# Kernel optimization log

Hardware: AMD Instinct MI355X
Metric: run time of the kernel (lower is better)

## Reference

```python
import jax, jax.numpy as jnp
import numpy as np

B, L, D = 2, 1024, 1024
H, KV, CH = 16, 4, 8          # attn heads, kv heads, context-manager heads
HD = D // H                   # 64
E, K, FF = 8, 2, 4 * D        # experts, top-k, ffn hidden
DC = 4                        # conv kernel size
EPS = 1e-6


def setup_inputs() -> dict:
    key = jax.random.key(0)
    ks = jax.random.split(key, 32)
    s = 0.02
    n = lambda k, shp: jax.random.normal(k, shp, jnp.float32) * s
    return {
        'x': jax.random.normal(ks[0], (B, L, D), jnp.float32),
        'mask': jnp.ones((B, L), jnp.int32),
        'w_rms1': jnp.ones((D,), jnp.float32),
        'w_rms2': jnp.ones((D,), jnp.float32),
        'w_rms3': jnp.ones((D,), jnp.float32),
        'w_rms4': jnp.ones((D,), jnp.float32),
        'Wq': n(ks[1], (D, D)), 'Wk': n(ks[2], (D, KV * HD)),
        'Wv': n(ks[3], (D, KV * HD)), 'Wo': n(ks[4], (D, D)),
        'Cq': n(ks[5], (D, D)), 'Ck': n(ks[6], (D, D)),
        'Cv': n(ks[7], (D, D)), 'Co': n(ks[8], (D, D)),
        'Wi': n(ks[9], (D, 2 * D)), 'bi': jnp.zeros((2 * D,), jnp.float32),
        'conv_w': n(ks[10], (D, 1, DC)), 'conv_b': jnp.zeros((D,), jnp.float32),
        'Wod': n(ks[11], (D, D)), 'bod': jnp.zeros((D,), jnp.float32),
        'w_gate': n(ks[12], (E, D)),
        'W1': n(ks[13], (E, D, FF)), 'b1': jnp.zeros((E, FF), jnp.float32),
        'W2': n(ks[14], (E, FF, D)), 'b2': jnp.zeros((E, D), jnp.float32),
    }


def _rmsnorm(x, w):
    rms = jnp.sqrt(jnp.mean(x * x, axis=-1, keepdims=True) + EPS)
    return w * (x / rms)


def _mha(x, mask, Wq, Wk, Wv, Wo, nh, nkv):
    b, l, d = x.shape
    hd = d // nh
    q = (x @ Wq).reshape(b, l, nh, hd)
    k = (x @ Wk).reshape(b, l, nkv, hd)
    v = (x @ Wv).reshape(b, l, nkv, hd)
    if nh != nkv:
        rep = nh // nkv
        k = jnp.repeat(k, rep, axis=2)
        v = jnp.repeat(v, rep, axis=2)
    scores = jnp.einsum('bqhd,bkhd->bhqk', q, k) * (hd ** -0.5)
    scores = jnp.where(mask[:, None, None, :] == 0, -jnp.inf, scores)
    attn = jax.nn.softmax(scores, axis=-1)
    out = jnp.einsum('bhqk,bkhd->bqhd', attn, v).reshape(b, l, d)
    return out @ Wo


def _deltanet(x, Wi, bi, conv_w, conv_b, Wod, bod):
    gv = x @ Wi + bi
    gate, value = jnp.split(gv, 2, axis=-1)
    # depthwise causal conv1d (kernel DC, left pad DC-1, truncated to L)
    v_ncl = jnp.transpose(value, (0, 2, 1))  # [B, D, L]
    conv = jax.lax.conv_general_dilated(
        v_ncl, conv_w, window_strides=(1,), padding=[(DC - 1, 0)],
        feature_group_count=D, dimension_numbers=('NCH', 'OIH', 'NCH'))
    conv = conv + conv_b[None, :, None]
    conv = jnp.transpose(conv, (0, 2, 1))  # [B, L, D]
    gated = conv * jax.nn.silu(gate)
    return gated @ Wod + bod


def _moe(x, w_gate, W1, b1, W2, b2):
    b, l, d = x.shape
    flat = x.reshape(-1, d)                                  # [T, D]
    gate = jax.nn.softmax(flat @ w_gate.T, axis=-1)          # [T, E]
    topk_scores, topk_idx = jax.lax.top_k(gate, K)           # [T, K]
    onehot = jax.nn.one_hot(topk_idx, E, dtype=flat.dtype)   # [T, K, E]
    combine = jnp.sum(topk_scores[..., None] * onehot, axis=1)  # [T, E]
    h = jnp.einsum('td,edh->teh', flat, W1) + b1
    h = jax.nn.gelu(h, approximate=False)
    y = jnp.einsum('teh,ehd->ted', h, W2) + b2
    out = jnp.einsum('ted,te->td', y, combine)
    return out.reshape(b, l, d)


def reference(x, mask, w_rms1, w_rms2, w_rms3, w_rms4,
              Wq, Wk, Wv, Wo, Cq, Ck, Cv, Co,
              Wi, bi, conv_w, conv_b, Wod, bod,
              w_gate, W1, b1, W2, b2):
    # eval mode: dropout = identity. multi_token_pred output is discarded by the block.
    res1 = x
    h = _rmsnorm(x, w_rms1)
    h = res1 + _mha(h, mask, Wq, Wk, Wv, Wo, H, KV)
    res2 = h
    # ContextManager stand-in: 8-head softmax self-attention (source unavailable)
    cm = _mha(h, mask, Cq, Ck, Cv, Co, CH, CH)
    h = res2 + cm
    res3 = h
    g = _rmsnorm(h, w_rms2)
    h = res3 + _deltanet(g, Wi, bi, conv_w, conv_b, Wod, bod)
    res4 = h
    g = _rmsnorm(h, w_rms3)
    h = res4 + _moe(g, w_gate, W1, b1, W2, b2)
    h = _rmsnorm(h, w_rms4)
    return h
```

## Files before the change

### kernel.cpp

```cpp
#include <hip/hip_runtime.h>
#include <hip/hip_bf16.h>
#include <math.h>

#define T_TOK 2048
#define B_SZ 2
#define L_SEQ 1024
#define D_MOD 1024
#define N_H 16
#define N_KV 4
#define N_CH 8
#define N_E 8
#define FF_DIM 4096
#define DC_K 4
#define EPS_F 1e-6f

typedef unsigned short u16;
typedef unsigned int u32;
typedef short s16x8 __attribute__((ext_vector_type(8)));
typedef u16 u16x8 __attribute__((ext_vector_type(8)));
typedef float f32x4 __attribute__((ext_vector_type(4)));
struct alignas(8) U16x4 { u16 a, b, c, d; };

__device__ __forceinline__ float gelu_exact(float x) {
    return 0.5f * x * (1.0f + erff(x * 0.70710678118654752f));
}
__device__ __forceinline__ u16 f2bf(float f) {
    u32 x = __float_as_uint(f);
    return (u16)((x + 0x7fffu + ((x >> 16) & 1u)) >> 16);
}
__device__ __forceinline__ float b2f(u16 u) {
    return __uint_as_float(((u32)u) << 16);
}
__device__ __forceinline__ void gload_lds16(const u16* g, u16* l) {
    __builtin_amdgcn_global_load_lds(
        (const __attribute__((address_space(1))) u32*)g,
        (__attribute__((address_space(3))) u32*)l, 16, 0, 0);
}

struct TDesc {
    const float* src;
    u16* dst;
    int R, C, dstStride, dstRowOff, tileBase, nPerMat;
};
struct TPack { TDesc d[12]; };

__global__ __launch_bounds__(256) void transpose_all(TPack p, int nTiles) {
    __shared__ float ts[64][65];
    int tid = threadIdx.x;
    int t = blockIdx.x;
    float4 rg[4];
    u16* dstB = nullptr;
    int dstStr = 0;

    auto prep = [&](int tt) {
        int i = 0;
#pragma unroll
        for (int j = 1; j < 12; ++j)
            if (tt >= p.d[j].tileBase) i = j;
        TDesc d = p.d[i];
        int local = tt - d.tileBase;
        int e = local / d.nPerMat;
        local -= e * d.nPerMat;
        int ntx = d.C >> 6;
        int bx = local % ntx, by = local / ntx;
        const float* src = d.src + (size_t)e * d.R * d.C + (size_t)(by * 64) * d.C + bx * 64;
#pragma unroll
        for (int k = 0; k < 4; ++k) {
            int fidx = k * 256 + tid;
            int r = fidx >> 4, c4 = (fidx & 15) << 2;
            rg[k] = *(const float4*)(src + (size_t)r * d.C + c4);
        }
        dstB = d.dst + (size_t)e * d.C * d.dstStride +
               (size_t)(d.dstRowOff + bx * 64) * d.dstStride + by * 64;
        dstStr = d.dstStride;
    };

    if (t < nTiles) prep(t);
    for (; t < nTiles; t += gridDim.x) {
#pragma unroll
        for (int k = 0; k < 4; ++k) {
            int fidx = k * 256 + tid;
            int r = fidx >> 4, c4 = (fidx & 15) << 2;
            ts[r][c4] = rg[k].x;
            ts[r][c4 + 1] = rg[k].y;
            ts[r][c4 + 2] = rg[k].z;
            ts[r][c4 + 3] = rg[k].w;
        }
        u16* db = dstB;
        int dstr = dstStr;
        __syncthreads();
        int tn = t + gridDim.x;
        if (tn < nTiles) prep(tn);
#pragma unroll
        for (int k = 0; k < 2; ++k) {
            int idx = k * 256 + tid;
            int c = idx >> 3, r8 = (idx & 7) << 3;
            u16x8 o;
#pragma unroll
            for (int j = 0; j < 8; ++j) o[j] = f2bf(ts[r8 + j][c]);
            *(u16x8*)(db + (size_t)c * dstr + r8) = o;
        }
        __syncthreads();
    }
}

__global__ __launch_bounds__(256) void rmsnorm_kernel(const float* __restrict__ x,
                                                      const float* __restrict__ w,
                                                      float* __restrict__ fo,
                                                      u16* __restrict__ bo) {
    int row = blockIdx.x;
    int tid = threadIdx.x;
    const float* xr = x + (size_t)row * D_MOD;
    float4 v = ((const float4*)xr)[tid];
    float ss = v.x * v.x + v.y * v.y + v.z * v.z + v.w * v.w;
    __shared__ float red[256];
    red[tid] = ss;
    __syncthreads();
    for (int s = 128; s > 0; s >>= 1) {
        if (tid < s) red[tid] += red[tid + s];
        __syncthreads();
    }
    float inv = 1.0f / sqrtf(red[0] * (1.0f / D_MOD) + EPS_F);
    float4 wv = ((const float4*)w)[tid];
    float4 o;
    o.x = v.x * inv * wv.x;
    o.y = v.y * inv * wv.y;
    o.z = v.z * inv * wv.z;
    o.w = v.w * inv * wv.w;
    if (fo) ((float4*)(fo + (size_t)row * D_MOD))[tid] = o;
    if (bo) {
        U16x4 b;
        b.a = f2bf(o.x); b.b = f2bf(o.y); b.c = f2bf(o.z); b.d = f2bf(o.w);
        *(U16x4*)(bo + (size_t)row * D_MOD + tid * 4) = b;
    }
}

template <int MODE, int GELU, int OUTF, int OUTB, int BM>
__global__ __launch_bounds__(256) void mfma_gemm(const u16* __restrict__ A,
                                                 const u16* __restrict__ BT,
                                                 const float* __restrict__ bias,
                                                 const float* __restrict__ res,
                                                 float* __restrict__ C,
                                                 u16* __restrict__ Cb,
                                                 const int* __restrict__ list,
                                                 const int* __restrict__ offs,
                                                 const int* __restrict__ counts,
                                                 int M, int N, int K, int nx) {
    constexpr int PWR = BM / 2;
    constexpr int MI = PWR / 16;
    constexpr int NI = 4;
    constexpr int NAI = (BM >= 64) ? (BM / 64) : 1;
    __shared__ u16 ldsA[2][BM * 32];
    __shared__ u16 ldsB[2][128 * 32];
    int tid = threadIdx.x;
    int lane = tid & 63, w = tid >> 6;
    int wr = w >> 1, wc = w & 1;
    int bx, by, e;
    if (MODE == 0) {
        bx = blockIdx.x; by = blockIdx.y; e = 0;
    } else {
        int id = blockIdx.x;
        e = id & 7;
        int r = id >> 3;
        bx = r % nx;
        by = r / nx;
    }
    int cnt, off;
    if (MODE == 0) { cnt = M; off = 0; }
    else { cnt = counts[e]; off = offs[e]; }
    int m0 = by * BM;
    if (m0 >= cnt) return;
    int n0 = bx * 128;
    const u16* Bt = BT + (size_t)e * (size_t)N * K;

    const u16* aSrc[NAI];
    const u16* bSrc[2];
#pragma unroll
    for (int j = 0; j < NAI; ++j) {
        int rowA = (BM >= 64) ? (j * 64 + w * 16 + (lane >> 2))
                              : (w * 16 + (lane >> 2));
        int slot = lane & 3;
        int rl = m0 + ((rowA < BM) ? rowA : (BM - 1));
        if (rl >= cnt) rl = cnt - 1;
        size_t ga;
        if (MODE == 1) ga = (size_t)list[off + rl] * K;
        else if (MODE == 2) ga = (size_t)(off + rl) * K;
        else ga = (size_t)rl * K;
        aSrc[j] = A + ga + ((slot ^ ((rowA >> 1) & 3)) << 3);
    }
#pragma unroll
    for (int j = 0; j < 2; ++j) {
        int rowB = j * 64 + w * 16 + (lane >> 2);
        int slot = lane & 3;
        bSrc[j] = Bt + (size_t)(n0 + rowB) * K + ((slot ^ ((rowB >> 1) & 3)) << 3);
    }

    auto stage = [&](int buf, int k0) {
        if constexpr (BM == 32) {
            if (w < 2) gload_lds16(aSrc[0] + k0, &ldsA[buf][w * 512]);
        } else {
#pragma unroll
            for (int j = 0; j < NAI; ++j)
                gload_lds16(aSrc[j] + k0, &ldsA[buf][(j * 256 + w * 64) * 8]);
        }
#pragma unroll
        for (int j = 0; j < 2; ++j)
            gload_lds16(bSrc[j] + k0, &ldsB[buf][(j * 256 + w * 64) * 8]);
    };

    f32x4 acc[MI][NI] = {};
    int r16 = lane & 15, cr = lane >> 4;

    stage(0, 0);
    __syncthreads();
    int cur = 0;
    for (int k0 = 0; k0 < K; k0 += 32) {
        if (k0 + 32 < K) stage(cur ^ 1, k0 + 32);
        s16x8 af[MI], bfr[NI];
#pragma unroll
        for (int mi = 0; mi < MI; ++mi) {
            int row = wr * PWR + mi * 16 + r16;
            af[mi] = *(const s16x8*)&ldsA[cur][row * 32 + ((cr ^ ((row >> 1) & 3)) << 3)];
        }
#pragma unroll
        for (int ni = 0; ni < NI; ++ni) {
            int row = wc * 64 + ni * 16 + r16;
            bfr[ni] = *(const s16x8*)&ldsB[cur][row * 32 + ((cr ^ ((row >> 1) & 3)) << 3)];
        }
#pragma unroll
        for (int mi = 0; mi < MI; ++mi)
#pragma unroll
            for (int ni = 0; ni < NI; ++ni)
                acc[mi][ni] = __builtin_amdgcn_mfma_f32_16x16x32_bf16(af[mi], bfr[ni],
                                                                      acc[mi][ni], 0, 0, 0);
        __syncthreads();
        cur ^= 1;
    }

    const float* bias_e = bias ? (bias + (MODE ? (size_t)e * N : 0)) : nullptr;
#pragma unroll
    for (int mi = 0; mi < MI; ++mi) {
#pragma unroll
        for (int ni = 0; ni < NI; ++ni) {
            int rloc = wr * PWR + mi * 16 + (lane >> 4) * 4;
            int col = n0 + wc * 64 + ni * 16 + (lane & 15);
#pragma unroll
            for (int jj = 0; jj < 4; ++jj) {
                int rl = m0 + rloc + jj;
                if (rl >= cnt) continue;
                float val = acc[mi][ni][jj];
                if (bias_e) val += bias_e[col];
                if (GELU) val = gelu_exact(val);
                size_t crow = (MODE == 0) ? (size_t)rl : (size_t)(off + rl);
                if (res) val += res[crow * N + col];
                if (OUTF) C[crow * N + col] = val;
                if (OUTB) Cb[crow * N + col] = f2bf(val);
            }
        }
    }
}

template <int HD>
__global__ __launch_bounds__(256) void mfma_attn(const u16* __restrict__ Qb,
                                                 const u16* __restrict__ Kb,
                                                 const u16* __restrict__ Vb,
                                                 u16* __restrict__ O,
                                                 int stride, int ostride,
                                                 int nh, int nkv, float scale) {
    constexpr int KT = 64;
    constexpr int CH = HD / 8;
    constexpr int NF = HD / 32;
    constexpr int ND = HD / 16;
    constexpr int VSTR = 72;
    constexpr int NISS = (64 * CH) / (64 * 4);

    __shared__ u16 Kl[64 * HD];
    __shared__ u16 Vt[HD * VSTR];
    __shared__ u16 Pl[4][16 * 72];

    int tid = threadIdx.x, lane = tid & 63, w = tid >> 6;
    int g = lane >> 4, r16 = lane & 15;
    int q0 = blockIdx.x * 64, h = blockIdx.y, b = blockIdx.z;
    int kvh = h / (nh / nkv);

    const u16* Qp = Qb + (size_t)(b * L_SEQ + q0 + w * 16 + r16) * stride + h * HD + g * 8;
    s16x8 qf[NF];
#pragma unroll
    for (int f = 0; f < NF; ++f) qf[f] = *(const s16x8*)(Qp + f * 32);

    const u16* Kbase = Kb + (size_t)(b * L_SEQ) * stride + (size_t)kvh * HD;
    const u16* Vbase = Vb + (size_t)(b * L_SEQ) * stride + (size_t)kvh * HD;

    int srcOffK[NISS];
#pragma unroll
    for (int i = 0; i < NISS; ++i) {
        int ci = (w * NISS + i) * 64 + lane;
        int row = ci / CH;
        int ch = ci % CH;
        srcOffK[i] = row * stride + ((ch ^ (row & 7)) << 3);
    }

    f32x4 ofr[ND] = {};
    float m_r[4], l_r[4];
#pragma unroll
    for (int r = 0; r < 4; ++r) { m_r[r] = -1e30f; l_r[r] = 0.f; }

    for (int kt = 0; kt < L_SEQ / KT; ++kt) {
        const u16* Ksrc = Kbase + (size_t)(kt * KT) * stride;
        const u16* Vsrc = Vbase + (size_t)(kt * KT) * stride;
        __syncthreads();
#pragma unroll
        for (int i = 0; i < NISS; ++i)
            gload_lds16(Ksrc + srcOffK[i], Kl + (size_t)(w * NISS + i) * 512);
#pragma unroll
        for (int half = 0; half < HD / 64; ++half) {
            int dbase = w * 16 + half * 64;
            u16x8 v0 = *(const u16x8*)(Vsrc + (size_t)lane * stride + dbase);
            u16x8 v1 = *(const u16x8*)(Vsrc + (size_t)lane * stride + dbase + 8);
#pragma unroll
            for (int j = 0; j < 8; ++j) {
                Vt[(dbase + j) * VSTR + lane] = v0[j];
                Vt[(dbase + 8 + j) * VSTR + lane] = v1[j];
            }
        }
        __syncthreads();

        f32x4 s[4];
        __builtin_amdgcn_s_setprio(1);
#pragma unroll
        for (int sub = 0; sub < 4; ++sub) {
            f32x4 acc = {};
#pragma unroll
            for (int f = 0; f < NF; ++f) {
                int row = sub * 16 + r16;
                int chunk = (f * 4 + g) ^ (row & 7);
                s16x8 kf = *(const s16x8*)&Kl[(row * CH + chunk) * 8];
                acc = __builtin_amdgcn_mfma_f32_16x16x32_bf16(qf[f], kf, acc, 0, 0, 0);
            }
            s[sub] = acc;
        }
        __builtin_amdgcn_s_setprio(0);

#pragma unroll
        for (int sub = 0; sub < 4; ++sub)
#pragma unroll
            for (int r = 0; r < 4; ++r) s[sub][r] *= scale;
#pragma unroll
        for (int r = 0; r < 4; ++r) {
            float mx = fmaxf(fmaxf(s[0][r], s[1][r]), fmaxf(s[2][r], s[3][r]));
            mx = fmaxf(mx, __shfl_xor(mx, 1));
            mx = fmaxf(mx, __shfl_xor(mx, 2));
            mx = fmaxf(mx, __shfl_xor(mx, 4));
            mx = fmaxf(mx, __shfl_xor(mx, 8));
            float mo = m_r[r];
            float mn = fmaxf(mo, mx);
            float sc = __expf(mo - mn);
            m_r[r] = mn;
            float sum = 0.f;
#pragma unroll
            for (int sub = 0; sub < 4; ++sub) {
                float e = __expf(s[sub][r] - mn);
                s[sub][r] = e;
                sum += e;
            }
            sum += __shfl_xor(sum, 1);
            sum += __shfl_xor(sum, 2);
            sum += __shfl_xor(sum, 4);
            sum += __shfl_xor(sum, 8);
            l_r[r] = l_r[r] * sc + sum;
#pragma unroll
            for (int dsub = 0; dsub < ND; ++dsub) ofr[dsub][r] *= sc;
        }

        u16* Pw = Pl[w];
#pragma unroll
        for (int sub = 0; sub < 4; ++sub)
#pragma unroll
            for (int r = 0; r < 4; ++r) {
                int q = g * 4 + r;
                int k = sub * 16 + r16;
                Pw[q * 72 + (((k >> 3) ^ (q & 7)) << 3) + (k & 7)] = f2bf(s[sub][r]);
            }
        __syncthreads();

        s16x8 pf[2];
#pragma unroll
        for (int ks = 0; ks < 2; ++ks) {
            int chunk = (ks * 4 + g) ^ (r16 & 7);
            pf[ks] = *(const s16x8*)&Pw[r16 * 72 + chunk * 8];
        }
        __builtin_amdgcn_s_setprio(1);
#pragma unroll
        for (int dsub = 0; dsub < ND; ++dsub)
#pragma unroll
            for (int ks = 0; ks < 2; ++ks) {
                s16x8 vf = *(const s16x8*)&Vt[(dsub * 16 + r16) * VSTR + ks * 32 + g * 8];
                ofr[dsub] = __builtin_amdgcn_mfma_f32_16x16x32_bf16(pf[ks], vf, ofr[dsub], 0, 0, 0);
            }
        __builtin_amdgcn_s_setprio(0);
    }

    float inv[4];
#pragma unroll
    for (int r = 0; r < 4; ++r) inv[r] = 1.0f / l_r[r];
#pragma unroll
    for (int dsub = 0; dsub < ND; ++dsub)
#pragma unroll
        for (int r = 0; r < 4; ++r) {
            int q = q0 + w * 16 + g * 4 + r;
            O[(size_t)(b * L_SEQ + q) * ostride + h * HD + dsub * 16 + r16] =
                f2bf(ofr[dsub][r] * inv[r]);
        }
}

__global__ __launch_bounds__(256) void conv_gate_kernel(const u16* __restrict__ gv,
                                                        const float* __restrict__ cw,
                                                        const float* __restrict__ cb,
                                                        u16* __restrict__ gated) {
    int idx = blockIdx.x * 256 + threadIdx.x;
    if (idx >= T_TOK * D_MOD / 8) return;
    int d8 = (idx & 127) << 3;
    int t = idx >> 7;
    int l = t & (L_SEQ - 1);
    float conv[8];
#pragma unroll
    for (int j = 0; j < 8; ++j) conv[j] = cb[d8 + j];
#pragma unroll
    for (int i = 0; i < DC_K; ++i) {
        int lp = l - (DC_K - 1) + i;
        if (lp >= 0) {
            u16x8 v8 = *(const u16x8*)(gv + (size_t)(t - l + lp) * (2 * D_MOD) + D_MOD + d8);
#pragma unroll
            for (int j = 0; j < 8; ++j) conv[j] += b2f(v8[j]) * cw[(d8 + j) * DC_K + i];
        }
    }
    u16x8 g8 = *(const u16x8*)(gv + (size_t)t * (2 * D_MOD) + d8);
    u16x8 o;
#pragma unroll
    for (int j = 0; j < 8; ++j) {
        float gate = b2f(g8[j]);
        float sig = 1.0f / (1.0f + expf(-gate));
        o[j] = f2bf(conv[j] * (gate * sig));
    }
    *(u16x8*)(gated + (size_t)t * D_MOD + d8) = o;
}

__global__ __launch_bounds__(256) void route_kernel(const float* __restrict__ g,
                                                    const float* __restrict__ wg,
                                                    int* __restrict__ tIdx,
                                                    float* __restrict__ tScore,
                                                    int* __restrict__ counts) {
    int t = blockIdx.x, tid = threadIdx.x;
    __shared__ float gs[D_MOD];
    __shared__ float logits[N_E];
    ((float4*)gs)[tid] = ((const float4*)(g + (size_t)t * D_MOD))[tid];
    __syncthreads();
    int e = tid >> 5, lane = tid & 31;
    const float* w = wg + (size_t)e * D_MOD;
    float p = 0.f;
    for (int d = lane; d < D_MOD; d += 32) p += gs[d] * w[d];
    for (int o = 16; o > 0; o >>= 1) p += __shfl_down(p, o, 32);
    if (lane == 0) logits[e] = p;
    __syncthreads();
    if (tid == 0) {
        float mx = logits[0];
        for (int e2 = 1; e2 < N_E; ++e2) mx = fmaxf(mx, logits[e2]);
        float pe[N_E];
        float Z = 0.f;
        for (int e2 = 0; e2 < N_E; ++e2) {
            pe[e2] = expf(logits[e2] - mx);
            Z += pe[e2];
        }
        int i0 = 0;
        float b0 = pe[0];
        for (int e2 = 1; e2 < N_E; ++e2)
            if (pe[e2] > b0) { b0 = pe[e2]; i0 = e2; }
        int i1 = -1;
        float b1 = -1.f;
        for (int e2 = 0; e2 < N_E; ++e2)
            if (e2 != i0 && pe[e2] > b1) { b1 = pe[e2]; i1 = e2; }
        float invZ = 1.0f / Z;
        tIdx[t * 2] = i0;
        tIdx[t * 2 + 1] = i1;
        tScore[t * 2] = b0 * invZ;
        tScore[t * 2 + 1] = b1 * invZ;
        atomicAdd(&counts[i0], 1);
        atomicAdd(&counts[i1], 1);
    }
}

__global__ void prefix_kernel(const int* __restrict__ counts, int* __restrict__ offs,
                              int* __restrict__ cursor) {
    if (threadIdx.x == 0) {
        int acc = 0;
        for (int e = 0; e < N_E; ++e) {
            offs[e] = acc;
            acc += counts[e];
            cursor[e] = 0;
        }
    }
}

__global__ __launch_bounds__(256) void fill_kernel(const int* __restrict__ tIdx,
                                                   const int* __restrict__ offs,
                                                   int* __restrict__ cursor,
                                                   int* __restrict__ list,
                                                   int* __restrict__ pairRow) {
    int t = blockIdx.x * 256 + threadIdx.x;
    if (t >= T_TOK) return;
    for (int kk = 0; kk < 2; ++kk) {
        int e = tIdx[t * 2 + kk];
        int pos = atomicAdd(&cursor[e], 1);
        int slot = offs[e] + pos;
        list[slot] = t;
        pairRow[t * 2 + kk] = slot;
    }
}

__global__ __launch_bounds__(256) void combine_rms_kernel(const u16* __restrict__ ysel,
                                                          const float* __restrict__ tScore,
                                                          const int* __restrict__ pairRow,
                                                          const float* __restrict__ h,
                                                          const float* __restrict__ w,
                                                          float* __restrict__ out) {
    int row = blockIdx.x;
    int tid = threadIdx.x;
    float4 v = ((const float4*)(h + (size_t)row * D_MOD))[tid];
    int r0 = pairRow[row * 2], r1 = pairRow[row * 2 + 1];
    float s0 = tScore[row * 2], s1 = tScore[row * 2 + 1];
    U16x4 y0 = *(const U16x4*)(ysel + (size_t)r0 * D_MOD + tid * 4);
    U16x4 y1 = *(const U16x4*)(ysel + (size_t)r1 * D_MOD + tid * 4);
    v.x += s0 * b2f(y0.a) + s1 * b2f(y1.a);
    v.y += s0 * b2f(y0.b) + s1 * b2f(y1.b);
    v.z += s0 * b2f(y0.c) + s1 * b2f(y1.c);
    v.w += s0 * b2f(y0.d) + s1 * b2f(y1.d);
    __shared__ float red[256];
    red[tid] = v.x * v.x + v.y * v.y + v.z * v.z + v.w * v.w;
    __syncthreads();
    for (int s = 128; s > 0; s >>= 1) {
        if (tid < s) red[tid] += red[tid + s];
        __syncthreads();
    }
    float inv = 1.0f / sqrtf(red[0] * (1.0f / D_MOD) + EPS_F);
    float4 wv = ((const float4*)w)[tid];
    float4 o;
    o.x = v.x * inv * wv.x;
    o.y = v.y * inv * wv.y;
    o.z = v.z * inv * wv.z;
    o.w = v.w * inv * wv.w;
    ((float4*)(out + (size_t)row * D_MOD))[tid] = o;
}

extern "C" void kernel_launch(void* const* d_in, const int* in_sizes, int n_in,
                              void* d_out, int out_size, void* d_ws, size_t ws_size,
                              hipStream_t stream) {
    const float* x = (const float*)d_in[0];
    const float* w_rms1 = (const float*)d_in[2];
    const float* w_rms2 = (const float*)d_in[3];
    const float* w_rms3 = (const float*)d_in[4];
    const float* w_rms4 = (const float*)d_in[5];
    const float* Wq = (const float*)d_in[6];
    const float* Wk = (const float*)d_in[7];
    const float* Wv = (const float*)d_in[8];
    const float* Wo = (const float*)d_in[9];
    const float* Cq = (const float*)d_in[10];
    const float* Ck = (const float*)d_in[11];
    const float* Cv = (const float*)d_in[12];
    const float* Co = (const float*)d_in[13];
    const float* Wi = (const float*)d_in[14];
    const float* bi = (const float*)d_in[15];
    const float* conv_w = (const float*)d_in[16];
    const float* conv_b = (const float*)d_in[17];
    const float* Wod = (const float*)d_in[18];
    const float* bod = (const float*)d_in[19];
    const float* w_gate = (const float*)d_in[20];
    const float* W1 = (const float*)d_in[21];
    const float* b1 = (const float*)d_in[22];
    const float* W2 = (const float*)d_in[23];
    const float* b2 = (const float*)d_in[24];
    float* out = (float*)d_out;

    char* ws = (char*)d_ws;
    size_t off = 0;
    auto alloc_f = [&](size_t n) { float* p = (float*)(ws + off); off += n * 4; return p; };
    auto alloc_b = [&](size_t n) { u16* p = (u16*)(ws + off); off += n * 2; return p; };

    u16* qkvT = alloc_b((size_t)1536 * 1024);
    u16* cqkvT = alloc_b((size_t)3072 * 1024);
    u16* WoT = alloc_b((size_t)1024 * 1024);
    u16* CoT = alloc_b((size_t)1024 * 1024);
    u16* WiT = alloc_b((size_t)2048 * 1024);
    u16* WodT = alloc_b((size_t)1024 * 1024);
    u16* W1T = alloc_b((size_t)N_E * FF_DIM * 1024);
    u16* W2T = alloc_b((size_t)N_E * 1024 * FF_DIM);
    const size_t TD = (size_t)T_TOK * D_MOD;
    float* h = alloc_f(TD);
    float* nrm = alloc_f(TD);
    u16* nrm_bf = alloc_b(TD);
    u16* h_bf = alloc_b(TD);
    u16* ab_bf = alloc_b(TD);
    u16* qkv_bf = alloc_b((size_t)T_TOK * 3072);
    u16* gv_bf = alloc_b((size_t)T_TOK * 2048);
    u16* hsel = alloc_b((size_t)2 * T_TOK * FF_DIM);
    u16* ysel = alloc_b((size_t)2 * T_TOK * D_MOD);
    int* counts = (int*)(ws + off); off += N_E * 4;
    int* offs = (int*)(ws + off); off += N_E * 4;
    int* cursor = (int*)(ws + off); off += N_E * 4;
    int* tIdx = (int*)(ws + off); off += 2 * T_TOK * 4;
    int* list = (int*)(ws + off); off += 2 * T_TOK * 4;
    int* pairRow = (int*)(ws + off); off += 2 * T_TOK * 4;
    float* tScore = alloc_f(2 * T_TOK);

    TPack tp;
    int tb = 0;
    auto mkd = [&](int i, const float* s, u16* d, int R, int C, int ds, int ro, int nmat) {
        int per = (C >> 6) * (R >> 6);
        tp.d[i] = TDesc{s, d, R, C, ds, ro, tb, per};
        tb += per * nmat;
    };
    mkd(0, Wq, qkvT, 1024, 1024, 1024, 0, 1);
    mkd(1, Wk, qkvT, 1024, 256, 1024, 1024, 1);
    mkd(2, Wv, qkvT, 1024, 256, 1024, 1280, 1);
    mkd(3, Cq, cqkvT, 1024, 1024, 1024, 0, 1);
    mkd(4, Ck, cqkvT, 1024, 1024, 1024, 1024, 1);
    mkd(5, Cv, cqkvT, 1024, 1024, 1024, 2048, 1);
    mkd(6, Wo, WoT, 1024, 1024, 1024, 0, 1);
    mkd(7, Co, CoT, 1024, 1024, 1024, 0, 1);
    mkd(8, Wi, WiT, 1024, 2048, 1024, 0, 1);
    mkd(9, Wod, WodT, 1024, 1024, 1024, 0, 1);
    mkd(10, W1, W1T, 1024, FF_DIM, 1024, 0, N_E);
    mkd(11, W2, W2T, FF_DIM, 1024, FF_DIM, 0, N_E);
    transpose_all<<<2048, 256, 0, stream>>>(tp, tb);

    rmsnorm_kernel<<<T_TOK, 256, 0, stream>>>(x, w_rms1, nullptr, nrm_bf);
    mfma_gemm<0, 0, 0, 1, 32><<<dim3(12, 64, 1), 256, 0, stream>>>(
        nrm_bf, qkvT, nullptr, nullptr, nullptr, qkv_bf, nullptr, nullptr, nullptr,
        T_TOK, 1536, 1024, 0);
    mfma_attn<64><<<dim3(16, N_H, B_SZ), 256, 0, stream>>>(
        qkv_bf, qkv_bf + 1024, qkv_bf + 1280, ab_bf, 1536, 1024, N_H, N_KV, 0.125f);
    mfma_gemm<0, 0, 1, 1, 32><<<dim3(8, 64, 1), 256, 0, stream>>>(
        ab_bf, WoT, nullptr, x, h, h_bf, nullptr, nullptr, nullptr, T_TOK, 1024, 1024, 0);

    mfma_gemm<0, 0, 0, 1, 32><<<dim3(24, 64, 1), 256, 0, stream>>>(
        h_bf, cqkvT, nullptr, nullptr, nullptr, qkv_bf, nullptr, nullptr, nullptr,
        T_TOK, 3072, 1024, 0);
    mfma_attn<128><<<dim3(16, N_CH, B_SZ), 256, 0, stream>>>(
        qkv_bf, qkv_bf + 1024, qkv_bf + 2048, ab_bf, 3072, 1024, N_CH, N_CH,
        0.088388347648318447f);
    mfma_gemm<0, 0, 1, 0, 32><<<dim3(8, 64, 1), 256, 0, stream>>>(
        ab_bf, CoT, nullptr, h, h, nullptr, nullptr, nullptr, nullptr, T_TOK, 1024, 1024, 0);

    rmsnorm_kernel<<<T_TOK, 256, 0, stream>>>(h, w_rms2, nullptr, nrm_bf);
    mfma_gemm<0, 0, 0, 1, 32><<<dim3(16, 64, 1), 256, 0, stream>>>(
        nrm_bf, WiT, bi, nullptr, nullptr, gv_bf, nullptr, nullptr, nullptr, T_TOK, 2048, 1024, 0);
    conv_gate_kernel<<<(T_TOK * D_MOD / 8 + 255) / 256, 256, 0, stream>>>(gv_bf, conv_w, conv_b, ab_bf);
    mfma_gemm<0, 0, 1, 0, 32><<<dim3(8, 64, 1), 256, 0, stream>>>(
        ab_bf, WodT, bod, h, h, nullptr, nullptr, nullptr, nullptr, T_TOK, 1024, 1024, 0);

    rmsnorm_kernel<<<T_TOK, 256, 0, stream>>>(h, w_rms3, nrm, nrm_bf);
    hipMemsetAsync(counts, 0, N_E * sizeof(int), stream);
    route_kernel<<<T_TOK, 256, 0, stream>>>(nrm, w_gate, tIdx, tScore, counts);
    prefix_kernel<<<1, 64, 0, stream>>>(counts, offs, cursor);
    fill_kernel<<<(T_TOK + 255) / 256, 256, 0, stream>>>(tIdx, offs, cursor, list, pairRow);
    mfma_gemm<1, 1, 0, 1, 128><<<32 * 16 * 8, 256, 0, stream>>>(
        nrm_bf, W1T, b1, nullptr, nullptr, hsel, list, offs, counts, T_TOK, FF_DIM, 1024, 32);
    mfma_gemm<2, 0, 0, 1, 32><<<8 * 64 * 8, 256, 0, stream>>>(
        hsel, W2T, b2, nullptr, nullptr, ysel, list, offs, counts, T_TOK, 1024, FF_DIM, 8);
    combine_rms_kernel<<<T_TOK, 256, 0, stream>>>(ysel, tScore, pairRow, h, w_rms4, out);
}
```

Baseline: 650.6 us.

## Spread expert weight transposes across dense GEMM kernels as tail work

Takes the MoE W1/W2 fp32→bf16 transposes out of the upfront transpose kernel and splits their 16384 tiles across the five dense GEMM launches. Each GEMM block does its tile after finishing its matmul output, reusing the same shared memory. The aim is to fill idle slots left by the small dense GEMM grids so the large expert transpose is no longer a serial launch on its own. The trade-off is longer GEMM kernels and a larger shared memory footprint when the transpose buffer is bigger than the GEMM tiles. The hard-coded tile ranges must also add up exactly to the full set.

```diff
diff --git a/kernel.cpp b/kernel.cpp
--- a/kernel.cpp
+++ b/kernel.cpp
@@ -42,65 +42,41 @@
     u16* dst;
     int R, C, dstStride, dstRowOff, tileBase, nPerMat;
 };
-struct TPack { TDesc d[12]; };
-
-__global__ __launch_bounds__(256) void transpose_all(TPack p, int nTiles) {
+struct TPack { TDesc d[10]; };
+
+__global__ __launch_bounds__(256) void transpose_all(TPack p) {
     __shared__ float ts[64][65];
+    int t = blockIdx.x;
+    int i = 0;
+#pragma unroll
+    for (int j = 1; j < 10; ++j)
+        if (t >= p.d[j].tileBase) i = j;
+    TDesc d = p.d[i];
+    int local = t - d.tileBase;
+    int e = local / d.nPerMat;
+    local -= e * d.nPerMat;
+    int ntx = d.C >> 6;
+    int bx = local % ntx, by = local / ntx;
+    const float* src = d.src + (size_t)e * d.R * d.C + (size_t)(by * 64) * d.C + bx * 64;
+    u16* dst = d.dst + (size_t)e * d.C * d.dstStride +
+               (size_t)(d.dstRowOff + bx * 64) * d.dstStride + by * 64;
     int tid = threadIdx.x;
-    int t = blockIdx.x;
-    float4 rg[4];
-    u16* dstB = nullptr;
-    int dstStr = 0;
-
-    auto prep = [&](int tt) {
-        int i = 0;
-#pragma unroll
-        for (int j = 1; j < 12; ++j)
-            if (tt >= p.d[j].tileBase) i = j;
-        TDesc d = p.d[i];
-        int local = tt - d.tileBase;
-        int e = local / d.nPerMat;
-        local -= e * d.nPerMat;
-        int ntx = d.C >> 6;
-        int bx = local % ntx, by = local / ntx;
-        const float* src = d.src + (size_t)e * d.R * d.C + (size_t)(by * 64) * d.C + bx * 64;
-#pragma unroll
-        for (int k = 0; k < 4; ++k) {
-            int fidx = k * 256 + tid;
-            int r = fidx >> 4, c4 = (fidx & 15) << 2;
-            rg[k] = *(const float4*)(src + (size_t)r * d.C + c4);
-        }
-        dstB = d.dst + (size_t)e * d.C * d.dstStride +
-               (size_t)(d.dstRowOff + bx * 64) * d.dstStride + by * 64;
-        dstStr = d.dstStride;
-    };
-
-    if (t < nTiles) prep(t);
-    for (; t < nTiles; t += gridDim.x) {
-#pragma unroll
-        for (int k = 0; k < 4; ++k) {
-            int fidx = k * 256 + tid;
-            int r = fidx >> 4, c4 = (fidx & 15) << 2;
-            ts[r][c4] = rg[k].x;
-            ts[r][c4 + 1] = rg[k].y;
-            ts[r][c4 + 2] = rg[k].z;
-            ts[r][c4 + 3] = rg[k].w;
-        }
-        u16* db = dstB;
-        int dstr = dstStr;
-        __syncthreads();
-        int tn = t + gridDim.x;
-        if (tn < nTiles) prep(tn);
-#pragma unroll
-        for (int k = 0; k < 2; ++k) {
-            int idx = k * 256 + tid;
-            int c = idx >> 3, r8 = (idx & 7) << 3;
-            u16x8 o;
-#pragma unroll
-            for (int j = 0; j < 8; ++j) o[j] = f2bf(ts[r8 + j][c]);
-            *(u16x8*)(db + (size_t)c * dstr + r8) = o;
-        }
-        __syncthreads();
+#pragma unroll
+    for (int k = 0; k < 4; ++k) {
+        int fidx = k * 256 + tid;
+        int r = fidx >> 4, c4 = (fidx & 15) << 2;
+        float4 v = *(const float4*)(src + (size_t)r * d.C + c4);
+        ts[r][c4] = v.x; ts[r][c4 + 1] = v.y; ts[r][c4 + 2] = v.z; ts[r][c4 + 3] = v.w;
+    }
+    __syncthreads();
+#pragma unroll
+    for (int k = 0; k < 2; ++k) {
+        int idx = k * 256 + tid;
+        int c = idx >> 3, r8 = (idx & 7) << 3;
+        u16x8 o;
+#pragma unroll
+        for (int j = 0; j < 8; ++j) o[j] = f2bf(ts[r8 + j][c]);
+        *(u16x8*)(dst + (size_t)c * d.dstStride + r8) = o;
     }
 }
 
@@ -135,7 +111,7 @@
     }
 }
 
-template <int MODE, int GELU, int OUTF, int OUTB, int BM>
+template <int MODE, int GELU, int OUTF, int OUTB, int BM, int TW>
 __global__ __launch_bounds__(256) void mfma_gemm(const u16* __restrict__ A,
                                                  const u16* __restrict__ BT,
                                                  const float* __restrict__ bias,
@@ -145,13 +121,22 @@
                                                  const int* __restrict__ list,
                                                  const int* __restrict__ offs,
                                                  const int* __restrict__ counts,
-                                                 int M, int N, int K, int nx) {
+                                                 int M, int N, int K, int nx,
+                                                 const float* __restrict__ tW1,
+                                                 const float* __restrict__ tW2,
+                                                 u16* __restrict__ tW1T,
+                                                 u16* __restrict__ tW2T,
+                                                 int tLo, int tHi) {
     constexpr int PWR = BM / 2;
     constexpr int MI = PWR / 16;
     constexpr int NI = 4;
     constexpr int NAI = (BM >= 64) ? (BM / 64) : 1;
-    __shared__ u16 ldsA[2][BM * 32];
-    __shared__ u16 ldsB[2][128 * 32];
+    constexpr int SMG = (2 * BM * 32 + 2 * 128 * 32) * 2;
+    constexpr int SMT = TW ? (64 * 65 * 4) : 0;
+    constexpr int SM = SMG > SMT ? SMG : SMT;
+    __shared__ alignas(16) char smem[SM];
+    u16* ldsA = (u16*)smem;
+    u16* ldsB = ldsA + 2 * BM * 32;
     int tid = threadIdx.x;
     int lane = tid & 63, w = tid >> 6;
     int wr = w >> 1, wc = w & 1;
@@ -169,93 +154,140 @@
     if (MODE == 0) { cnt = M; off = 0; }
     else { cnt = counts[e]; off = offs[e]; }
     int m0 = by * BM;
-    if (m0 >= cnt) return;
-    int n0 = bx * 128;
-    const u16* Bt = BT + (size_t)e * (size_t)N * K;
-
-    const u16* aSrc[NAI];
-    const u16* bSrc[2];
-#pragma unroll
-    for (int j = 0; j < NAI; ++j) {
-        int rowA = (BM >= 64) ? (j * 64 + w * 16 + (lane >> 2))
-                              : (w * 16 + (lane >> 2));
-        int slot = lane & 3;
-        int rl = m0 + ((rowA < BM) ? rowA : (BM - 1));
-        if (rl >= cnt) rl = cnt - 1;
-        size_t ga;
-        if (MODE == 1) ga = (size_t)list[off + rl] * K;
-        else if (MODE == 2) ga = (size_t)(off + rl) * K;
-        else ga = (size_t)rl * K;
-        aSrc[j] = A + ga + ((slot ^ ((rowA >> 1) & 3)) << 3);
-    }
-#pragma unroll
-    for (int j = 0; j < 2; ++j) {
-        int rowB = j * 64 + w * 16 + (lane >> 2);
-        int slot = lane & 3;
-        bSrc[j] = Bt + (size_t)(n0 + rowB) * K + ((slot ^ ((rowB >> 1) & 3)) << 3);
-    }
-
-    auto stage = [&](int buf, int k0) {
-        if constexpr (BM == 32) {
-            if (w < 2) gload_lds16(aSrc[0] + k0, &ldsA[buf][w * 512]);
-        } else {
-#pragma unroll
-            for (int j = 0; j < NAI; ++j)
-                gload_lds16(aSrc[j] + k0, &ldsA[buf][(j * 256 + w * 64) * 8]);
-        }
-#pragma unroll
-        for (int j = 0; j < 2; ++j)
-            gload_lds16(bSrc[j] + k0, &ldsB[buf][(j * 256 + w * 64) * 8]);
-    };
-
-    f32x4 acc[MI][NI] = {};
-    int r16 = lane & 15, cr = lane >> 4;
-
-    stage(0, 0);
-    __syncthreads();
-    int cur = 0;
-    for (int k0 = 0; k0 < K; k0 += 32) {
-        if (k0 + 32 < K) stage(cur ^ 1, k0 + 32);
-        s16x8 af[MI], bfr[NI];
+    if (m0 < cnt) {
+        int n0 = bx * 128;
+        const u16* Bt = BT + (size_t)e * (size_t)N * K;
+
+        const u16* aSrc[NAI];
+        const u16* bSrc[2];
+#pragma unroll
+        for (int j = 0; j < NAI; ++j) {
+            int rowA = (BM >= 64) ? (j * 64 + w * 16 + (lane >> 2))
+                                  : (w * 16 + (lane >> 2));
+            int slot = lane & 3;
+            int rl = m0 + ((rowA < BM) ? rowA : (BM - 1));
+            if (rl >= cnt) rl = cnt - 1;
+            size_t ga;
+            if (MODE == 1) ga = (size_t)list[off + rl] * K;
+            else if (MODE == 2) ga = (size_t)(off + rl) * K;
+            else ga = (size_t)rl * K;
+            aSrc[j] = A + ga + ((slot ^ ((rowA >> 1) & 3)) << 3);
+        }
+#pragma unroll
+        for (int j = 0; j < 2; ++j) {
+            int rowB = j * 64 + w * 16 + (lane >> 2);
+            int slot = lane & 3;
+            bSrc[j] = Bt + (size_t)(n0 + rowB) * K + ((slot ^ ((rowB >> 1) & 3)) << 3);
+        }
+
+        auto stage = [&](int buf, int k0) {
+            if constexpr (BM == 32) {
+                if (w < 2) gload_lds16(aSrc[0] + k0, ldsA + buf * (BM * 32) + w * 512);
+            } else {
+#pragma unroll
+                for (int j = 0; j < NAI; ++j)
+                    gload_lds16(aSrc[j] + k0, ldsA + buf * (BM * 32) + (j * 256 + w * 64) * 8);
+            }
+#pragma unroll
+            for (int j = 0; j < 2; ++j)
+                gload_lds16(bSrc[j] + k0, ldsB + buf * 4096 + (j * 256 + w * 64) * 8);
+        };
+
+        f32x4 acc[MI][NI] = {};
+        int r16 = lane & 15, cr = lane >> 4;
+
+        stage(0, 0);
+        __syncthreads();
+        int cur = 0;
+        for (int k0 = 0; k0 < K; k0 += 32) {
+            if (k0 + 32 < K) stage(cur ^ 1, k0 + 32);
+            s16x8 af[MI], bfr[NI];
+#pragma unroll
+            for (int mi = 0; mi < MI; ++mi) {
+                int row = wr * PWR + mi * 16 + r16;
+                af[mi] = *(const s16x8*)&ldsA[cur * (BM * 32) + row * 32 +
+                                              ((cr ^ ((row >> 1) & 3)) << 3)];
+            }
+#pragma unroll
+            for (int ni = 0; ni < NI; ++ni) {
+                int row = wc * 64 + ni * 16 + r16;
+                bfr[ni] = *(const s16x8*)&ldsB[cur * 4096 + row * 32 +
+                                               ((cr ^ ((row >> 1) & 3)) << 3)];
+            }
+#pragma unroll
+            for (int mi = 0; mi < MI; ++mi)
+#pragma unroll
+                for (int ni = 0; ni < NI; ++ni)
+                    acc[mi][ni] = __builtin_amdgcn_mfma_f32_16x16x32_bf16(af[mi], bfr[ni],
+                                                                          acc[mi][ni], 0, 0, 0);
+            __syncthreads();
+            cur ^= 1;
+        }
+
+        const float* bias_e = bias ? (bias + (MODE ? (size_t)e * N : 0)) : nullptr;
 #pragma unroll
         for (int mi = 0; mi < MI; ++mi) {
-            int row = wr * PWR + mi * 16 + r16;
-            af[mi] = *(const s16x8*)&ldsA[cur][row * 32 + ((cr ^ ((row >> 1) & 3)) << 3)];
-        }
-#pragma unroll
-        for (int ni = 0; ni < NI; ++ni) {
-            int row = wc * 64 + ni * 16 + r16;
-            bfr[ni] = *(const s16x8*)&ldsB[cur][row * 32 + ((cr ^ ((row >> 1) & 3)) << 3)];
-        }
-#pragma unroll
-        for (int mi = 0; mi < MI; ++mi)
-#pragma unroll
-            for (int ni = 0; ni < NI; ++ni)
-                acc[mi][ni] = __builtin_amdgcn_mfma_f32_16x16x32_bf16(af[mi], bfr[ni],
-                                                                      acc[mi][ni], 0, 0, 0);
+#pragma unroll
+            for (int ni = 0; ni < NI; ++ni) {
+                int rloc = wr * PWR + mi * 16 + (lane >> 4) * 4;
+                int col = n0 + wc * 64 + ni * 16 + (lane & 15);
+#pragma unroll
+                for (int jj = 0; jj < 4; ++jj) {
+                    int rl = m0 + rloc + jj;
+                    if (rl >= cnt) continue;
+                    float val = acc[mi][ni][jj];
+                    if (bias_e) val += bias_e[col];
+                    if (GELU) val = gelu_exact(val);
+                    size_t crow = (MODE == 0) ? (size_t)rl : (size_t)(off + rl);
+                    if (res) val += res[crow * N + col];
+                    if (OUTF) C[crow * N + col] = val;
+                    if (OUTB) Cb[crow * N + col] = f2bf(val);
+                }
+            }
+        }
+    }
+
+    if constexpr (TW) {
+        int nb = gridDim.x * gridDim.y;
+        int bid = blockIdx.y * gridDim.x + blockIdx.x;
+        float (*ts)[65] = (float(*)[65])smem;
         __syncthreads();
-        cur ^= 1;
-    }
-
-    const float* bias_e = bias ? (bias + (MODE ? (size_t)e * N : 0)) : nullptr;
-#pragma unroll
-    for (int mi = 0; mi < MI; ++mi) {
-#pragma unroll
-        for (int ni = 0; ni < NI; ++ni) {
-            int rloc = wr * PWR + mi * 16 + (lane >> 4) * 4;
-            int col = n0 + wc * 64 + ni * 16 + (lane & 15);
-#pragma unroll
-            for (int jj = 0; jj < 4; ++jj) {
-                int rl = m0 + rloc + jj;
-                if (rl >= cnt) continue;
-                float val = acc[mi][ni][jj];
-                if (bias_e) val += bias_e[col];
-                if (GELU) val = gelu_exact(val);
-                size_t crow = (MODE == 0) ? (size_t)rl : (size_t)(off + rl);
-                if (res) val += res[crow * N + col];
-                if (OUTF) C[crow * N + col] = val;
-                if (OUTB) Cb[crow * N + col] = f2bf(val);
-            }
+        for (int t = tLo + bid; t < tHi; t += nb) {
+            const float* src;
+            u16* dst;
+            int Cc, ds;
+            if (t < 8192) {
+                int ee = t >> 10, loc = t & 1023;
+                int tbx = loc & 63, tby = loc >> 6;
+                src = tW1 + (size_t)ee * 1024 * FF_DIM + (size_t)(tby << 6) * FF_DIM + (tbx << 6);
+                dst = tW1T + (size_t)ee * FF_DIM * 1024 + (size_t)(tbx << 6) * 1024 + (tby << 6);
+                Cc = FF_DIM; ds = 1024;
+            } else {
+                int tt = t - 8192;
+                int ee = tt >> 10, loc = tt & 1023;
+                int tbx = loc & 15, tby = loc >> 4;
+                src = tW2 + (size_t)ee * FF_DIM * 1024 + (size_t)(tby << 6) * 1024 + (tbx << 6);
+                dst = tW2T + (size_t)ee * 1024 * FF_DIM + (size_t)(tbx << 6) * FF_DIM + (tby << 6);
+                Cc = 1024; ds = FF_DIM;
+            }
+#pragma unroll
+            for (int k = 0; k < 4; ++k) {
+                int fidx = k * 256 + tid;
+                int r = fidx >> 4, c4 = (fidx & 15) << 2;
+                float4 v = *(const float4*)(src + (size_t)r * Cc + c4);
+                ts[r][c4] = v.x; ts[r][c4 + 1] = v.y; ts[r][c4 + 2] = v.z; ts[r][c4 + 3] = v.w;
+            }
+            __syncthreads();
+#pragma unroll
+            for (int k = 0; k < 2; ++k) {
+                int idx = k * 256 + tid;
+                int c = idx >> 3, r8 = (idx & 7) << 3;
+                u16x8 o;
+#pragma unroll
+                for (int j = 0; j < 8; ++j) o[j] = f2bf(ts[r8 + j][c]);
+                *(u16x8*)(dst + (size_t)c * ds + r8) = o;
+            }
+            __syncthreads();
         }
     }
 }
@@ -613,58 +645,62 @@
 
     TPack tp;
     int tb = 0;
-    auto mkd = [&](int i, const float* s, u16* d, int R, int C, int ds, int ro, int nmat) {
+    auto mkd = [&](int i, const float* s, u16* d, int R, int C, int ds, int ro) {
         int per = (C >> 6) * (R >> 6);
         tp.d[i] = TDesc{s, d, R, C, ds, ro, tb, per};
-        tb += per * nmat;
+        tb += per;
     };
-    mkd(0, Wq, qkvT, 1024, 1024, 1024, 0, 1);
-    mkd(1, Wk, qkvT, 1024, 256, 1024, 1024, 1);
-    mkd(2, Wv, qkvT, 1024, 256, 1024, 1280, 1);
-    mkd(3, Cq, cqkvT, 1024, 1024, 1024, 0, 1);
-    mkd(4, Ck, cqkvT, 1024, 1024, 1024, 1024, 1);
-    mkd(5, Cv, cqkvT, 1024, 1024, 1024, 2048, 1);
-    mkd(6, Wo, WoT, 1024, 1024, 1024, 0, 1);
-    mkd(7, Co, CoT, 1024, 1024, 1024, 0, 1);
-    mkd(8, Wi, WiT, 1024, 2048, 1024, 0, 1);
-    mkd(9, Wod, WodT, 1024, 1024, 1024, 0, 1);
-    mkd(10, W1, W1T, 1024, FF_DIM, 1024, 0, N_E);
-    mkd(11, W2, W2T, FF_DIM, 1024, FF_DIM, 0, N_E);
-    transpose_all<<<2048, 256, 0, stream>>>(tp, tb);
+    mkd(0, Wq, qkvT, 1024, 1024, 1024, 0);
+    mkd(1, Wk, qkvT, 1024, 256, 1024, 1024);
+    mkd(2, Wv, qkvT, 1024, 256, 1024, 1280);
+    mkd(3, Cq, cqkvT, 1024, 1024, 1024, 0);
+    mkd(4, Ck, cqkvT, 1024, 1024, 1024, 1024);
+    mkd(5, Cv, cqkvT, 1024, 1024, 1024, 2048);
+    mkd(6, Wo, WoT, 1024, 1024, 1024, 0);
+    mkd(7, Co, CoT, 1024, 1024, 1024, 0);
+    mkd(8, Wi, WiT, 1024, 2048, 1024, 0);
+    mkd(9, Wod, WodT, 1024, 1024, 1024, 0);
+    transpose_all<<<tb, 256, 0, stream>>>(tp);
 
     rmsnorm_kernel<<<T_TOK, 256, 0, stream>>>(x, w_rms1, nullptr, nrm_bf);
-    mfma_gemm<0, 0, 0, 1, 32><<<dim3(12, 64, 1), 256, 0, stream>>>(
+    mfma_gemm<0, 0, 0, 1, 32, 1><<<dim3(12, 64, 1), 256, 0, stream>>>(
         nrm_bf, qkvT, nullptr, nullptr, nullptr, qkv_bf, nullptr, nullptr, nullptr,
-        T_TOK, 1536, 1024, 0);
+        T_TOK, 1536, 1024, 0, W1, W2, W1T, W2T, 0, 2600);
     mfma_attn<64><<<dim3(16, N_H, B_SZ), 256, 0, stream>>>(
         qkv_bf, qkv_bf + 1024, qkv_bf + 1280, ab_bf, 1536, 1024, N_H, N_KV, 0.125f);
-    mfma_gemm<0, 0, 1, 1, 32><<<dim3(8, 64, 1), 256, 0, stream>>>(
-        ab_bf, WoT, nullptr, x, h, h_bf, nullptr, nullptr, nullptr, T_TOK, 1024, 1024, 0);
-
-    mfma_gemm<0, 0, 0, 1, 32><<<dim3(24, 64, 1), 256, 0, stream>>>(
+    mfma_gemm<0, 0, 1, 1, 32, 1><<<dim3(8, 64, 1), 256, 0, stream>>>(
+        ab_bf, WoT, nullptr, x, h, h_bf, nullptr, nullptr, nullptr,
+        T_TOK, 1024, 1024, 0, W1, W2, W1T, W2T, 2600, 4300);
+
+    mfma_gemm<0, 0, 0, 1, 32, 1><<<dim3(24, 64, 1), 256, 0, stream>>>(
         h_bf, cqkvT, nullptr, nullptr, nullptr, qkv_bf, nullptr, nullptr, nullptr,
-        T_TOK, 3072, 1024, 0);
+        T_TOK, 3072, 1024, 0, W1, W2, W1T, W2T, 4300, 9500);
     mfma_attn<128><<<dim3(16, N_CH, B_SZ), 256, 0, stream>>>(
         qkv_bf, qkv_bf + 1024, qkv_bf + 2048, ab_bf, 3072, 1024, N_CH, N_CH,
         0.088388347648318447f);
-    mfma_gemm<0, 0, 1, 0, 32><<<dim3(8, 64, 1), 256, 0, stream>>>(
-        ab_bf, CoT, nullptr, h, h, nullptr, nullptr, nullptr, nullptr, T_TOK, 1024, 1024, 0);
+    mfma_gemm<0, 0, 1, 0, 32, 1><<<dim3(8, 64, 1), 256, 0, stream>>>(
+        ab_bf, CoT, nullptr, h, h, nullptr, nullptr, nullptr, nullptr,
+        T_TOK, 1024, 1024, 0, W1, W2, W1T, W2T, 9500, 11200);
 
     rmsnorm_kernel<<<T_TOK, 256, 0, stream>>>(h, w_rms2, nullptr, nrm_bf);
-    mfma_gemm<0, 0, 0, 1, 32><<<dim3(16, 64, 1), 256, 0, stream>>>(
-        nrm_bf, WiT, bi, nullptr, nullptr, gv_bf, nullptr, nullptr, nullptr, T_TOK, 2048, 1024, 0);
+    mfma_gemm<0, 0, 0, 1, 32, 1><<<dim3(16, 64, 1), 256, 0, stream>>>(
+        nrm_bf, WiT, bi, nullptr, nullptr, gv_bf, nullptr, nullptr, nullptr,
+        T_TOK, 2048, 1024, 0, W1, W2, W1T, W2T, 11200, 14684);
     conv_gate_kernel<<<(T_TOK * D_MOD / 8 + 255) / 256, 256, 0, stream>>>(gv_bf, conv_w, conv_b, ab_bf);
-    mfma_gemm<0, 0, 1, 0, 32><<<dim3(8, 64, 1), 256, 0, stream>>>(
-        ab_bf, WodT, bod, h, h, nullptr, nullptr, nullptr, nullptr, T_TOK, 1024, 1024, 0);
+    mfma_gemm<0, 0, 1, 0, 32, 1><<<dim3(8, 64, 1), 256, 0, stream>>>(
+        ab_bf, WodT, bod, h, h, nullptr, nullptr, nullptr, nullptr,
+        T_TOK, 1024, 1024, 0, W1, W2, W1T, W2T, 14684, 16384);
 
     rmsnorm_kernel<<<T_TOK, 256, 0, stream>>>(h, w_rms3, nrm, nrm_bf);
     hipMemsetAsync(counts, 0, N_E * sizeof(int), stream);
     route_kernel<<<T_TOK, 256, 0, stream>>>(nrm, w_gate, tIdx, tScore, counts);
     prefix_kernel<<<1, 64, 0, stream>>>(counts, offs, cursor);
     fill_kernel<<<(T_TOK + 255) / 256, 256, 0, stream>>>(tIdx, offs, cursor, list, pairRow);
-    mfma_gemm<1, 1, 0, 1, 128><<<32 * 16 * 8, 256, 0, stream>>>(
-        nrm_bf, W1T, b1, nullptr, nullptr, hsel, list, offs, counts, T_TOK, FF_DIM, 1024, 32);
-    mfma_gemm<2, 0, 0, 1, 32><<<8 * 64 * 8, 256, 0, stream>>>(
-        hsel, W2T, b2, nullptr, nullptr, ysel, list, offs, counts, T_TOK, 1024, FF_DIM, 8);
+    mfma_gemm<1, 1, 0, 1, 128, 0><<<32 * 16 * 8, 256, 0, stream>>>(
+        nrm_bf, W1T, b1, nullptr, nullptr, hsel, list, offs, counts,
+        T_TOK, FF_DIM, 1024, 32, nullptr, nullptr, nullptr, nullptr, 0, 0);
+    mfma_gemm<2, 0, 0, 1, 32, 0><<<8 * 64 * 8, 256, 0, stream>>>(
+        hsel, W2T, b2, nullptr, nullptr, ysel, list, offs, counts,
+        T_TOK, 1024, FF_DIM, 8, nullptr, nullptr, nullptr, nullptr, 0, 0);
     combine_rms_kernel<<<T_TOK, 256, 0, stream>>>(ysel, tScore, pairRow, h, w_rms4, out);
 }
```

Result: faster. 632.4 us (-2.8%).
